# Kernel tuning notes

Measured on AMD Instinct MI355X. Metric: run time of the kernel, lower is better.

## Reference

```python
import jax, jax.numpy as jnp
import numpy as np

SIZE = 32          # resize target (self.size)
WIN = 11           # SSIM gaussian window
SIGMA = 1.5
THRESH = 0.3       # cal_thresh
C1 = (0.01 * 255.0) ** 2
C2 = (0.03 * 255.0) ** 2


def _gauss_kernel():
    x = jnp.arange(WIN, dtype=jnp.float32) - (WIN - 1) / 2.0
    g = jnp.exp(-(x ** 2) / (2.0 * SIGMA ** 2))
    g = g / g.sum()
    k = jnp.outer(g, g)
    return jnp.tile(k[None, None], (3, 1, 1, 1))  # [3,1,11,11] depthwise


def _dwconv(x, k):
    # x: [N,3,h,w] depthwise gaussian blur, SAME padding (pytorch-ssim style)
    return jax.lax.conv_general_dilated(x, k, (1, 1), 'SAME', feature_group_count=3)


def _crop_resize(img, box, H, W):
    # img [3,H,W], box cxcywh -> [3,SIZE,SIZE]; mimics int() crop + F.interpolate
    # (bilinear, align_corners=False)
    cx, cy, w, h = box[0], box[1], box[2], box[3]
    x0 = jnp.clip(jnp.floor(cx - w / 2), 0.0, W - 1.0)
    x1 = jnp.clip(jnp.floor(cx + w / 2), 0.0, float(W))
    y0 = jnp.clip(jnp.floor(cy - h / 2), 0.0, H - 1.0)
    y1 = jnp.clip(jnp.floor(cy + h / 2), 0.0, float(H))
    wp = jnp.maximum(x1 - x0, 1.0)  # crop width (>=1 to stay well-defined)
    hp = jnp.maximum(y1 - y0, 1.0)
    d = jnp.arange(SIZE, dtype=jnp.float32) + 0.5
    sx = x0 + jnp.clip(d * wp / SIZE - 0.5, 0.0, wp - 1.0)  # source cols
    sy = y0 + jnp.clip(d * hp / SIZE - 0.5, 0.0, hp - 1.0)  # source rows
    ix0 = jnp.floor(sx); iy0 = jnp.floor(sy)
    fx = sx - ix0; fy = sy - iy0
    ix0 = ix0.astype(jnp.int32); iy0 = iy0.astype(jnp.int32)
    ix1 = jnp.minimum(ix0 + 1, (x0 + wp - 1.0).astype(jnp.int32))
    iy1 = jnp.minimum(iy0 + 1, (y0 + hp - 1.0).astype(jnp.int32))

    def gat(iy, ix):
        return img[:, iy[:, None], ix[None, :]]  # [3,SIZE,SIZE]

    return (gat(iy0, ix0) * ((1 - fy)[None, :, None] * (1 - fx)[None, None, :])
            + gat(iy0, ix1) * ((1 - fy)[None, :, None] * fx[None, None, :])
            + gat(iy1, ix0) * (fy[None, :, None] * (1 - fx)[None, None, :])
            + gat(iy1, ix1) * (fy[None, :, None] * fx[None, None, :]))


def _pairwise_iou(gt, pr, eps=1e-16):
    # gt [B,Ng,4], pr [B,Np,4] cxcywh -> iou [B,Ng,Np] (same math as get_two_box_iou)
    g1, g2 = gt[:, :, None, :2], gt[:, :, None, 2:]
    p1, p2 = pr[:, None, :, :2], pr[:, None, :, 2:]
    tl = jnp.maximum(g1 - g2 / 2, p1 - p2 / 2)
    br = jnp.minimum(g1 + g2 / 2, p1 + p2 / 2)
    a_g = jnp.prod(gt[:, :, 2:], -1)[:, :, None]
    a_p = jnp.prod(pr[:, :, 2:], -1)[:, None, :]
    en = jnp.prod((tl < br).astype(gt.dtype), -1)
    a_i = jnp.prod(br - tl, -1) * en
    return a_i / (a_g + a_p - a_i + eps)


def _forward(imgs, gt_boxes, pred_boxes):
    B, C, H, W = imgs.shape
    Ng, Np = gt_boxes.shape[1], pred_boxes.shape[1]
    iou = _pairwise_iou(gt_boxes, pred_boxes)                        # [B,Ng,Np]
    valid = ((iou > THRESH)
             & (pred_boxes[:, None, :, 2] > 2)
             & (pred_boxes[:, None, :, 3] > 2))
    crop = jax.vmap(lambda im, bx: jax.vmap(lambda b: _crop_resize(im, b, H, W))(bx))
    g = crop(imgs, gt_boxes)    # [B,Ng,3,32,32]
    p = crop(imgs, pred_boxes)  # [B,Np,3,32,32]

    k = _gauss_kernel()
    mu_g = _dwconv(g.reshape(B * Ng, 3, SIZE, SIZE), k).reshape(B, Ng, 3, SIZE, SIZE)
    mu_p = _dwconv(p.reshape(B * Np, 3, SIZE, SIZE), k).reshape(B, Np, 3, SIZE, SIZE)
    sig_g = _dwconv((g * g).reshape(B * Ng, 3, SIZE, SIZE), k).reshape(B, Ng, 3, SIZE, SIZE) - mu_g ** 2
    sig_p = _dwconv((p * p).reshape(B * Np, 3, SIZE, SIZE), k).reshape(B, Np, 3, SIZE, SIZE) - mu_p ** 2

    gp = g[:, :, None] * p[:, None, :]                               # [B,Ng,Np,3,32,32]
    mug = mu_g[:, :, None]; mup = mu_p[:, None, :]
    sig_gp = _dwconv(gp.reshape(B * Ng * Np, 3, SIZE, SIZE), k).reshape(B, Ng, Np, 3, SIZE, SIZE) - mug * mup
    ssim_map = ((2 * mug * mup + C1) * (2 * sig_gp + C2)) / ((mug ** 2 + mup ** 2 + C1) * (sig_g[:, :, None] + sig_p[:, None, :] + C2))
    ssim_pair = ssim_map.mean(axis=(-3, -2, -1))                     # [B,Ng,Np]

    l1_pair = (jnp.abs(g[:, :, None] - p[:, None, :]) / 255.0).mean(axis=(-3, -2, -1))

    wv = valid.astype(imgs.dtype)
    cnt = wv.sum()
    mean_valid = lambda x: (x * wv).sum() / jnp.maximum(cnt, 1.0)
    # original: (L1(p/255,g/255) + SSIM_loss(p,g)).mean() over valid pairs
    loss = mean_valid(l1_pair) + (1.0 - mean_valid(ssim_pair))
    return jnp.where(cnt > 0, loss, jnp.zeros((), imgs.dtype))


def setup_inputs() -> dict:
    key = jax.random.key(0)
    k1, k2, k3, k4 = jax.random.split(key, 4)
    B, H, W, Ng, Np = 4, 640, 640, 16, 64
    imgs = jax.random.uniform(k1, (B, 3, H, W), jnp.float32, 0.0, 255.0)
    cxy = jax.random.uniform(k2, (B, Ng, 2), jnp.float32, 64.0, 576.0)
    wh = jax.random.uniform(k3, (B, Ng, 2), jnp.float32, 16.0, 128.0)
    gt_boxes = jnp.concatenate([cxy, wh], -1)
    # preds = jittered copies of GT so many pairs pass the IoU > 0.3 gate
    pred_boxes = jnp.tile(gt_boxes, (1, Np // Ng, 1)) + jax.random.normal(k4, (B, Np, 4), jnp.float32) * 4.0
    return {"imgs": imgs, "gt_boxes": gt_boxes, "pred_boxes": pred_boxes}


def reference(imgs, gt_boxes, pred_boxes):
    return _forward(imgs, gt_boxes, pred_boxes)
```

## Files before the change

kernel.cpp:

```cpp
#include <hip/hip_runtime.h>
#include <math.h>

#define WIN 11
#define HALF 5
#define SZ 32
#define PST 33
#define BB 4
#define NG 16
#define NP 64
#define IH 640
#define IW 640
#define NPIX 3072
#define NPAIR 4096
#define NSLOT 512
#define SSIM_C1 6.5025f
#define SSIM_C2 58.5225f

#define GW_INIT {0.001028379f, 0.007598757f, 0.036000791f, 0.109360748f, \
                 0.213005174f, 0.266011868f, 0.213005174f, 0.109360748f, \
                 0.036000791f, 0.007598757f, 0.001028379f}


__device__ __forceinline__ bool pair_valid(const float* __restrict__ gt,
                                           const float* __restrict__ pr, int idx) {
    int b = idx >> 10;
    int r = idx & 1023;
    int gi = r >> 6, pi = r & 63;
    const float* g = gt + (b * NG + gi) * 4;
    const float* p = pr + (b * NP + pi) * 4;
    float gx = g[0], gy = g[1], gw = g[2], gh = g[3];
    float px = p[0], py = p[1], pw = p[2], ph = p[3];
    float tlx = fmaxf(gx - gw * 0.5f, px - pw * 0.5f);
    float tly = fmaxf(gy - gh * 0.5f, py - ph * 0.5f);
    float brx = fminf(gx + gw * 0.5f, px + pw * 0.5f);
    float bry = fminf(gy + gh * 0.5f, py + ph * 0.5f);
    float en = ((tlx < brx) && (tly < bry)) ? 1.f : 0.f;
    float ai = (brx - tlx) * (bry - tly) * en;
    float iou = ai / (gw * gh + pw * ph - ai + 1e-16f);
    return (iou > 0.3f && pw > 2.f && ph > 2.f);
}

__global__ __launch_bounds__(256) void k_valid(const float* __restrict__ gt,
                                               const float* __restrict__ pr,
                                               int* __restrict__ list,
                                               int* __restrict__ count) {
    const int t = threadIdx.x;
    const int wave = t >> 6, lane = t & 63;
    __shared__ int s_wcnt[4];

    int cnt = 0;
#pragma unroll 1
    for (int i = 0; i < 16; ++i) {
        int idx = wave * 1024 + i * 64 + lane;
        unsigned long long m = __ballot(pair_valid(gt, pr, idx));
        cnt += __popcll(m);
    }
    if (lane == 0) s_wcnt[wave] = cnt;
    __syncthreads();

    int base = 0;
#pragma unroll
    for (int w = 0; w < 4; ++w)
        if (w < wave) base += s_wcnt[w];

#pragma unroll 1
    for (int i = 0; i < 16; ++i) {
        int idx = wave * 1024 + i * 64 + lane;
        bool v = pair_valid(gt, pr, idx);
        unsigned long long m = __ballot(v);
        if (v) list[base + __popcll(m & ((1ull << lane) - 1ull))] = idx;
        base += __popcll(m);
    }
    if (t == 0) *count = s_wcnt[0] + s_wcnt[1] + s_wcnt[2] + s_wcnt[3];
}

__device__ __forceinline__ void bilinear4(const float* __restrict__ ic,
                                          const float* __restrict__ box,
                                          int y, int xb, float out[4]) {
    float cx = box[0], cy = box[1], bw = box[2], bh = box[3];
    float x0 = fminf(fmaxf(floorf(cx - bw * 0.5f), 0.f), (float)(IW - 1));
    float x1 = fminf(fmaxf(floorf(cx + bw * 0.5f), 0.f), (float)IW);
    float y0 = fminf(fmaxf(floorf(cy - bh * 0.5f), 0.f), (float)(IH - 1));
    float y1 = fminf(fmaxf(floorf(cy + bh * 0.5f), 0.f), (float)IH);
    float wp = fmaxf(x1 - x0, 1.f);
    float hp = fmaxf(y1 - y0, 1.f);
    int xmax = (int)(x0 + wp - 1.f);
    int ymax = (int)(y0 + hp - 1.f);

    float sy = y0 + fminf(fmaxf(((float)y + 0.5f) * hp * (1.f / 32.f) - 0.5f, 0.f), hp - 1.f);
    float fly = floorf(sy);
    int iy0 = (int)fly;
    float fy = sy - fly;
    int iy1 = min(iy0 + 1, ymax);
    const float* r0 = ic + iy0 * IW;
    const float* r1 = ic + iy1 * IW;
#pragma unroll
    for (int j = 0; j < 4; ++j) {
        int x = xb + j;
        float sx = x0 + fminf(fmaxf(((float)x + 0.5f) * wp * (1.f / 32.f) - 0.5f, 0.f), wp - 1.f);
        float flx = floorf(sx);
        int ix0 = (int)flx;
        float fx = sx - flx;
        int ix1 = min(ix0 + 1, xmax);
        float v00 = r0[ix0], v01 = r0[ix1], v10 = r1[ix0], v11 = r1[ix1];
        out[j] = v00 * (1.f - fy) * (1.f - fx) + v01 * (1.f - fy) * fx +
                 v10 * fy * (1.f - fx) + v11 * fy * fx;
    }
}

__global__ __launch_bounds__(256) void k_all(const int* __restrict__ list,
                                             const int* __restrict__ count,
                                             const float* __restrict__ imgs,
                                             const float* __restrict__ gt,
                                             const float* __restrict__ pr,
                                             float* __restrict__ pairL1,
                                             float* __restrict__ pairSS) {
    const int c = blockIdx.x;
    const int n = *count;
    const int t = threadIdx.x;
    const int y = t >> 3;
    const int xb = (t & 7) * 4;
    const int wave = t >> 6, lane = t & 63;

    __shared__ float cg[SZ][PST];
    __shared__ float cp[SZ][PST];
    __shared__ float hg[SZ][PST];
    __shared__ float hg2[SZ][PST];
    __shared__ float hp_[SZ][PST];
    __shared__ float hp2[SZ][PST];
    __shared__ float hgp[SZ][PST];
    __shared__ float rl[4], rs[4];
    constexpr float GW[WIN] = GW_INIT;

    for (int slot = blockIdx.y; slot < n; slot += NSLOT) {
        const int pair = list[slot];
        const int b = pair >> 10;
        const int r = pair & 1023;
        const int gi = r >> 6, pi = r & 63;
        const float* gbox = gt + (b * NG + gi) * 4;
        const float* pbox = pr + (b * NP + pi) * 4;
        const float* ic = imgs + ((size_t)b * 3 + c) * IH * IW;

        float gv[4], pv[4];
        bilinear4(ic, gbox, y, xb, gv);
        bilinear4(ic, pbox, y, xb, pv);

        float l1 = 0.f;
#pragma unroll
        for (int j = 0; j < 4; ++j) {
            l1 += fabsf(gv[j] - pv[j]);
            cg[y][xb + j] = gv[j];
            cp[y][xb + j] = pv[j];
        }
        __syncthreads();

#pragma unroll
        for (int j = 0; j < 4; ++j) {
            int x = xb + j;
            float a1 = 0.f, a2 = 0.f, a3 = 0.f, a4 = 0.f, a5 = 0.f;
#pragma unroll
            for (int k = 0; k < WIN; ++k) {
                int xx = x + k - HALF;
                if (xx >= 0 && xx < SZ) {
                    float gval = cg[y][xx];
                    float pval = cp[y][xx];
                    a1 += GW[k] * gval;
                    a2 += GW[k] * gval * gval;
                    a3 += GW[k] * pval;
                    a4 += GW[k] * pval * pval;
                    a5 += GW[k] * gval * pval;
                }
            }
            hg[y][x] = a1;
            hg2[y][x] = a2;
            hp_[y][x] = a3;
            hp2[y][x] = a4;
            hgp[y][x] = a5;
        }
        __syncthreads();

        float ss = 0.f;
#pragma unroll
        for (int j = 0; j < 4; ++j) {
            int x = xb + j;
            float a1 = 0.f, a2 = 0.f, a3 = 0.f, a4 = 0.f, a5 = 0.f;
#pragma unroll
            for (int k = 0; k < WIN; ++k) {
                int yy = y + k - HALF;
                if (yy >= 0 && yy < SZ) {
                    a1 += GW[k] * hg[yy][x];
                    a2 += GW[k] * hg2[yy][x];
                    a3 += GW[k] * hp_[yy][x];
                    a4 += GW[k] * hp2[yy][x];
                    a5 += GW[k] * hgp[yy][x];
                }
            }
            float m1 = a1, m2 = a3;
            float sg = a2 - m1 * m1;
            float sp = a4 - m2 * m2;
            float sgp = a5 - m1 * m2;
            float num = (2.f * m1 * m2 + SSIM_C1) * (2.f * sgp + SSIM_C2);
            float den = (m1 * m1 + m2 * m2 + SSIM_C1) * (sg + sp + SSIM_C2);
            ss += num / den;
        }

#pragma unroll
        for (int off = 32; off > 0; off >>= 1) {
            l1 += __shfl_down(l1, off);
            ss += __shfl_down(ss, off);
        }
        if (lane == 0) { rl[wave] = l1; rs[wave] = ss; }
        __syncthreads();
        if (t == 0) {
            pairL1[slot * 3 + c] = rl[0] + rl[1] + rl[2] + rl[3];
            pairSS[slot * 3 + c] = rs[0] + rs[1] + rs[2] + rs[3];
        }
    }
}

__global__ __launch_bounds__(256) void k_final(const int* __restrict__ count,
                                               const float* __restrict__ pairL1,
                                               const float* __restrict__ pairSS,
                                               float* __restrict__ out) {
    const int n3 = (*count) * 3;
    const int t = threadIdx.x;
    float L = 0.f, S = 0.f;
    for (int i = t; i < n3; i += 256) {
        L += pairL1[i];
        S += pairSS[i];
    }
    __shared__ float rl[4], rs[4];
#pragma unroll
    for (int off = 32; off > 0; off >>= 1) {
        L += __shfl_down(L, off);
        S += __shfl_down(S, off);
    }
    const int wave = t >> 6, lane = t & 63;
    if (lane == 0) { rl[wave] = L; rs[wave] = S; }
    __syncthreads();
    if (t == 0) {
        float cnt = (float)(*count);
        float Lt = (rl[0] + rl[1] + rl[2] + rl[3]) * (1.0f / (255.0f * (float)NPIX));
        float St = (rs[0] + rs[1] + rs[2] + rs[3]) * (1.0f / (float)NPIX);
        float m = fmaxf(cnt, 1.f);
        float loss = Lt / m + 1.f - St / m;
        out[0] = (cnt > 0.f) ? loss : 0.f;
    }
}

extern "C" void kernel_launch(void* const* d_in, const int* in_sizes, int n_in,
                              void* d_out, int out_size, void* d_ws, size_t ws_size,
                              hipStream_t stream) {
    const float* imgs = (const float*)d_in[0];
    const float* gt = (const float*)d_in[1];
    const float* pr = (const float*)d_in[2];

    float* ws = (float*)d_ws;
    float* pairL1 = ws;
    float* pairSS = pairL1 + (size_t)NPAIR * 3;
    int* list = (int*)(pairSS + (size_t)NPAIR * 3);
    int* count = list + NPAIR;

    k_valid<<<1, 256, 0, stream>>>(gt, pr, list, count);
    k_all<<<dim3(3, NSLOT), 256, 0, stream>>>(list, count, imgs, gt, pr, pairL1, pairSS);
    k_final<<<1, 256, 0, stream>>>(count, pairL1, pairSS, (float*)d_out);
}
```

Baseline: 97.01 us.

## Precompute all box crops once and reuse them across valid pairs

Adds a first kernel that bilinearly resamples every GT and predicted box crop (320 crops × 3 channels) into workspace, with the pair-validity scan folded in as one extra block. The pair kernel then reads the precomputed 32x32 crops with vectorized loads instead of gathering from the full images for each pair. This removes repeated scattered gathers, since GT crops were redone for every matching prediction. In exchange it spends extra work on crops no valid pair uses and a round trip through global memory. The slot count is also reduced.

```diff
diff --git a/kernel.cpp b/kernel.cpp
--- a/kernel.cpp
+++ b/kernel.cpp
@@ -10,9 +10,11 @@
 #define NP 64
 #define IH 640
 #define IW 640
+#define CPIX 1024
 #define NPIX 3072
+#define NCROP 320
 #define NPAIR 4096
-#define NSLOT 512
+#define NSLOT 384
 #define SSIM_C1 6.5025f
 #define SSIM_C2 58.5225f
 
@@ -40,43 +42,55 @@
     return (iou > 0.3f && pw > 2.f && ph > 2.f);
 }
 
-__global__ __launch_bounds__(256) void k_valid(const float* __restrict__ gt,
-                                               const float* __restrict__ pr,
-                                               int* __restrict__ list,
-                                               int* __restrict__ count) {
+__global__ __launch_bounds__(256) void k_crop_valid(const float* __restrict__ imgs,
+                                                    const float* __restrict__ gt,
+                                                    const float* __restrict__ pr,
+                                                    float* __restrict__ crops,
+                                                    int* __restrict__ list,
+                                                    int* __restrict__ count) {
+    const int blk = blockIdx.x;
     const int t = threadIdx.x;
     const int wave = t >> 6, lane = t & 63;
-    __shared__ int s_wcnt[4];
-
-    int cnt = 0;
+
+    if (blk == 3 * NCROP) {
+        __shared__ int s_wcnt[4];
+        int cnt = 0;
 #pragma unroll 1
-    for (int i = 0; i < 16; ++i) {
-        int idx = wave * 1024 + i * 64 + lane;
-        unsigned long long m = __ballot(pair_valid(gt, pr, idx));
-        cnt += __popcll(m);
-    }
-    if (lane == 0) s_wcnt[wave] = cnt;
-    __syncthreads();
-
-    int base = 0;
-#pragma unroll
-    for (int w = 0; w < 4; ++w)
-        if (w < wave) base += s_wcnt[w];
-
+        for (int i = 0; i < 16; ++i) {
+            unsigned long long m = __ballot(pair_valid(gt, pr, wave * 1024 + i * 64 + lane));
+            cnt += __popcll(m);
+        }
+        if (lane == 0) s_wcnt[wave] = cnt;
+        __syncthreads();
+        int base = 0;
+#pragma unroll
+        for (int w = 0; w < 4; ++w)
+            if (w < wave) base += s_wcnt[w];
 #pragma unroll 1
-    for (int i = 0; i < 16; ++i) {
-        int idx = wave * 1024 + i * 64 + lane;
-        bool v = pair_valid(gt, pr, idx);
-        unsigned long long m = __ballot(v);
-        if (v) list[base + __popcll(m & ((1ull << lane) - 1ull))] = idx;
-        base += __popcll(m);
-    }
-    if (t == 0) *count = s_wcnt[0] + s_wcnt[1] + s_wcnt[2] + s_wcnt[3];
-}
-
-__device__ __forceinline__ void bilinear4(const float* __restrict__ ic,
-                                          const float* __restrict__ box,
-                                          int y, int xb, float out[4]) {
+        for (int i = 0; i < 16; ++i) {
+            int idx = wave * 1024 + i * 64 + lane;
+            bool v = pair_valid(gt, pr, idx);
+            unsigned long long m = __ballot(v);
+            if (v) list[base + __popcll(m & ((1ull << lane) - 1ull))] = idx;
+            base += __popcll(m);
+        }
+        if (t == 0) *count = s_wcnt[0] + s_wcnt[1] + s_wcnt[2] + s_wcnt[3];
+        return;
+    }
+
+    const int crop = blk / 3;
+    const int c = blk - crop * 3;
+    int b;
+    const float* box;
+    if (crop < BB * NG) {
+        b = crop >> 4;
+        box = gt + crop * 4;
+    } else {
+        int id = crop - BB * NG;
+        b = id >> 6;
+        box = pr + id * 4;
+    }
+
     float cx = box[0], cy = box[1], bw = box[2], bh = box[3];
     float x0 = fminf(fmaxf(floorf(cx - bw * 0.5f), 0.f), (float)(IW - 1));
     float x1 = fminf(fmaxf(floorf(cx + bw * 0.5f), 0.f), (float)IW);
@@ -87,13 +101,19 @@
     int xmax = (int)(x0 + wp - 1.f);
     int ymax = (int)(y0 + hp - 1.f);
 
+    const int y = t >> 3;
+    const int xb = (t & 7) * 4;
+
     float sy = y0 + fminf(fmaxf(((float)y + 0.5f) * hp * (1.f / 32.f) - 0.5f, 0.f), hp - 1.f);
     float fly = floorf(sy);
     int iy0 = (int)fly;
     float fy = sy - fly;
     int iy1 = min(iy0 + 1, ymax);
+
+    const float* ic = imgs + ((size_t)b * 3 + c) * IH * IW;
     const float* r0 = ic + iy0 * IW;
     const float* r1 = ic + iy1 * IW;
+    float vv[4];
 #pragma unroll
     for (int j = 0; j < 4; ++j) {
         int x = xb + j;
@@ -103,18 +123,18 @@
         float fx = sx - flx;
         int ix1 = min(ix0 + 1, xmax);
         float v00 = r0[ix0], v01 = r0[ix1], v10 = r1[ix0], v11 = r1[ix1];
-        out[j] = v00 * (1.f - fy) * (1.f - fx) + v01 * (1.f - fy) * fx +
-                 v10 * fy * (1.f - fx) + v11 * fy * fx;
-    }
-}
-
-__global__ __launch_bounds__(256) void k_all(const int* __restrict__ list,
-                                             const int* __restrict__ count,
-                                             const float* __restrict__ imgs,
-                                             const float* __restrict__ gt,
-                                             const float* __restrict__ pr,
-                                             float* __restrict__ pairL1,
-                                             float* __restrict__ pairSS) {
+        vv[j] = v00 * (1.f - fy) * (1.f - fx) + v01 * (1.f - fy) * fx +
+                v10 * fy * (1.f - fx) + v11 * fy * fx;
+    }
+    float* dst = crops + (size_t)crop * NPIX + c * CPIX + t * 4;
+    *(float4*)dst = make_float4(vv[0], vv[1], vv[2], vv[3]);
+}
+
+__global__ __launch_bounds__(256) void k_pair(const int* __restrict__ list,
+                                              const int* __restrict__ count,
+                                              const float* __restrict__ crops,
+                                              float* __restrict__ pairL1,
+                                              float* __restrict__ pairSS) {
     const int c = blockIdx.x;
     const int n = *count;
     const int t = threadIdx.x;
@@ -137,21 +157,17 @@
         const int b = pair >> 10;
         const int r = pair & 1023;
         const int gi = r >> 6, pi = r & 63;
-        const float* gbox = gt + (b * NG + gi) * 4;
-        const float* pbox = pr + (b * NP + pi) * 4;
-        const float* ic = imgs + ((size_t)b * 3 + c) * IH * IW;
-
-        float gv[4], pv[4];
-        bilinear4(ic, gbox, y, xb, gv);
-        bilinear4(ic, pbox, y, xb, pv);
-
-        float l1 = 0.f;
-#pragma unroll
-        for (int j = 0; j < 4; ++j) {
-            l1 += fabsf(gv[j] - pv[j]);
-            cg[y][xb + j] = gv[j];
-            cp[y][xb + j] = pv[j];
-        }
+        const size_t goff = (size_t)(b * NG + gi) * NPIX + c * CPIX;
+        const size_t poff = (size_t)(BB * NG + b * NP + pi) * NPIX + c * CPIX;
+
+        float4 gv = *(const float4*)(crops + goff + t * 4);
+        float4 pv = *(const float4*)(crops + poff + t * 4);
+        float l1 = fabsf(gv.x - pv.x) + fabsf(gv.y - pv.y) +
+                   fabsf(gv.z - pv.z) + fabsf(gv.w - pv.w);
+        cg[y][xb + 0] = gv.x; cp[y][xb + 0] = pv.x;
+        cg[y][xb + 1] = gv.y; cp[y][xb + 1] = pv.y;
+        cg[y][xb + 2] = gv.z; cp[y][xb + 2] = pv.z;
+        cg[y][xb + 3] = gv.w; cp[y][xb + 3] = pv.w;
         __syncthreads();
 
 #pragma unroll
@@ -256,12 +272,13 @@
     const float* pr = (const float*)d_in[2];
 
     float* ws = (float*)d_ws;
-    float* pairL1 = ws;
+    float* crops = ws;
+    float* pairL1 = crops + (size_t)NCROP * NPIX;
     float* pairSS = pairL1 + (size_t)NPAIR * 3;
     int* list = (int*)(pairSS + (size_t)NPAIR * 3);
     int* count = list + NPAIR;
 
-    k_valid<<<1, 256, 0, stream>>>(gt, pr, list, count);
-    k_all<<<dim3(3, NSLOT), 256, 0, stream>>>(list, count, imgs, gt, pr, pairL1, pairSS);
+    k_crop_valid<<<3 * NCROP + 1, 256, 0, stream>>>(imgs, gt, pr, crops, list, count);
+    k_pair<<<dim3(3, NSLOT), 256, 0, stream>>>(list, count, crops, pairL1, pairSS);
     k_final<<<1, 256, 0, stream>>>(count, pairL1, pairSS, (float*)d_out);
 }
```

Result: faster. 94.61 us (-2.5%).
